# Kernel optimization log

Measured on AMD Instinct MI355X. Metric: run time of the kernel, lower is better.

The kernel has to match this reference:

```python
import jax, jax.numpy as jnp
import numpy as np
from jax import lax

NEG = -1e9
B, H, C, TX, TY = 4, 256, 80, 256, 1024  # batch, hidden, mel bins, text len, mel len


def setup_inputs() -> dict:
    key = jax.random.key(0)
    k = jax.random.split(key, 6)
    en = jax.random.normal(k[0], (B, H, TX), jnp.float32)
    mu = jax.random.normal(k[1], (B, C, TX), jnp.float32)
    log_sigma = 0.1 * jax.random.normal(k[2], (B, C, TX), jnp.float32)
    y = jax.random.normal(k[3], (B, C, TY), jnp.float32)
    x_lengths = jax.random.randint(k[4], (B,), TX // 2, TX + 1, jnp.int32)
    y_lengths = jax.random.randint(k[5], (B,), TY // 2, TY + 1, jnp.int32)
    return {"en": en, "mu": mu, "log_sigma": log_sigma, "y": y,
            "x_lengths": x_lengths, "y_lengths": y_lengths}


def sequence_mask(lengths, max_len):
    return jnp.arange(max_len)[None, :] < lengths[:, None]


def compute_log_probs(mu, log_sigma, y):
    # y: [B,C,Ty] -> [B,1,Ty,C]; mu/log_sigma: [B,C,Tx] -> [B,Tx,1,C]
    yb = jnp.transpose(y, (0, 2, 1))[:, None]
    mub = jnp.transpose(mu, (0, 2, 1))[:, :, None]
    lsb = jnp.transpose(log_sigma, (0, 2, 1))[:, :, None]
    # mse / sigma^2 = (y-mu)^2 * exp(-2*log_sigma); mean over channel dim
    expo = -0.5 * jnp.mean((yb - mub) ** 2 * jnp.exp(-2.0 * lsb), axis=-1)  # [B,Tx,Ty]
    return expo - 0.5 * jnp.mean(lsb, axis=-1)  # broadcast [B,Tx,1] -> [B,Tx,Ty]


def maximum_path(logp, mask, x_lengths, y_lengths):
    """Monotonic alignment search (Glow-TTS Viterbi DP), vectorized over batch."""
    b, tx, ty = logp.shape
    lp = jnp.where(mask > 0, logp, NEG)
    cols = jnp.moveaxis(lp, 2, 0)  # [Ty, B, Tx]
    v0 = jnp.broadcast_to(jnp.where(jnp.arange(tx) == 0, 0.0, NEG), (b, tx)).astype(logp.dtype)

    def fwd(v, col):
        v_shift = jnp.concatenate([jnp.full((b, 1), NEG, v.dtype), v[:, :-1]], axis=1)
        diag = v_shift > v  # come from (x-1, y-1) rather than (x, y-1)
        return col + jnp.maximum(v, v_shift), diag

    _, diags = lax.scan(fwd, v0, cols)  # diags: [Ty, B, Tx] bool

    xs_idx = jnp.arange(tx)

    def bwd(idx, inp):
        yv, dcol = inp
        active = yv < y_lengths  # [B]
        row = (xs_idx[None, :] == idx[:, None]) & active[:, None]
        d = jnp.take_along_axis(dcol, idx[:, None], axis=1)[:, 0]
        idx = jnp.where(active & (idx > 0) & d, idx - 1, idx)
        return idx, row

    _, rows = lax.scan(bwd, x_lengths - 1, (jnp.arange(ty), diags), reverse=True)
    return lax.stop_gradient(jnp.moveaxis(rows, 0, 2).astype(logp.dtype))  # [B,Tx,Ty]


def generate_path(dr, mask):
    # dr: [B,Tx] durations; mask: [B,Tx,Ty]
    ty = mask.shape[-1]
    cum = jnp.cumsum(dr, axis=1)
    pm = (jnp.arange(ty)[None, None, :] < cum[:, :, None]).astype(dr.dtype)
    path = pm - jnp.pad(pm, ((0, 0), (1, 0), (0, 0)))[:, :-1]
    return path * mask


def reference(en, mu, log_sigma, y, x_lengths, y_lengths):
    tx, ty = mu.shape[-1], y.shape[-1]
    x_mask = sequence_mask(x_lengths, tx).astype(jnp.float32)  # [B,Tx]
    y_mask = sequence_mask(y_lengths, ty).astype(jnp.float32)  # [B,Ty]
    attn_mask = x_mask[:, :, None] * y_mask[:, None, :]        # [B,Tx,Ty]
    logp = compute_log_probs(mu, log_sigma, y)
    attn = maximum_path(logp, attn_mask, x_lengths, y_lengths)
    dr_mas = jnp.sum(attn, axis=-1)                            # durations [B,Tx]
    path = generate_path(dr_mas, attn_mask)                    # convert_dr_to_align
    # expand_encoder_outputs: attn^T @ en^T -> [B,H,Ty]
    o_en_ex = jnp.einsum('bxy,bhx->bhy', path, en)
    return o_en_ex, logp, attn, dr_mas
```

## Files before the change

### kernel.cpp

```cpp
#include <hip/hip_runtime.h>
#include <cstdint>
#include <cmath>

#define B_ 4
#define H_ 256
#define C_ 80
#define TX_ 256
#define TY_ 1024
#define NEGF (-1e9f)

#define OFF_LOGP (B_*H_*TY_)
#define OFF_ATTN (OFF_LOGP + B_*TX_*TY_)
#define OFF_DR   (OFF_ATTN + B_*TX_*TY_)

__device__ __forceinline__ float dpp_shr1_negfill_f32(float x) {
  union { float f; int i; } u, o, r;
  u.f = x; o.f = NEGF;
  r.i = __builtin_amdgcn_update_dpp(o.i, u.i, 0x138, 0xf, 0xf, false);
  return r.f;
}

__global__ __launch_bounds__(256) void k_logp(
    const float* __restrict__ mu, const float* __restrict__ ls,
    const float* __restrict__ y, const int* __restrict__ xlp,
    const int* __restrict__ ylp, float* __restrict__ logp_out,
    float* __restrict__ lpT)
{
  const int b  = blockIdx.z;
  const int tq = blockIdx.y;
  const int x0 = blockIdx.x * 4;
  const int tid = threadIdx.x;
  const int lane = tid & 63;
  const int xi = tid >> 6;

  __shared__ double2 s_wm[4][C_];
  __shared__ double  s_wm2[4][C_];
  __shared__ double  s_lsv[4][C_];
  __shared__ double  s_K[4];
  __shared__ double  s_t0[4];
  __shared__ float   tile[256][4];

  for (int i = tid; i < 4 * C_; i += 256) {
    int xj = i / C_, c = i - xj * C_;
    double m = (double)mu[(b * C_ + c) * TX_ + x0 + xj];
    double l = (double)ls[(b * C_ + c) * TX_ + x0 + xj];
    double w = exp(-2.0 * l);
    s_wm[xj][c]  = make_double2(w, -2.0 * w * m);
    s_wm2[xj][c] = w * m * m;
    s_lsv[xj][c] = l;
  }
  __syncthreads();
  {
    int cc = lane;
    double kp = (cc < C_) ? s_wm2[xi][cc] : 0.0;
    double tp = (cc < C_) ? s_lsv[xi][cc] : 0.0;
    if (cc + 64 < C_) { kp += s_wm2[xi][cc + 64]; tp += s_lsv[xi][cc + 64]; }
#pragma unroll
    for (int off = 32; off; off >>= 1) {
      kp += __shfl_down(kp, off);
      tp += __shfl_down(tp, off);
    }
    if (cc == 0) { s_K[xi] = kp; s_t0[xi] = -0.5 * (tp * (1.0 / C_)); }
  }
  __syncthreads();

  double acc[4];
#pragma unroll
  for (int k = 0; k < 4; ++k) acc[k] = 0.0;

  const float4* yp = (const float4*)(y + (size_t)b * C_ * TY_ + tq * 256) + lane;
#pragma unroll 4
  for (int c = 0; c < C_; ++c) {
    float4 yv = yp[c * (TY_ / 4)];
    double y0 = yv.x, y1 = yv.y, y2 = yv.z, y3 = yv.w;
    double2 wm = s_wm[xi][c];
    double w = wm.x, m1 = wm.y;
    double u0 = fma(w, y0, m1), u1 = fma(w, y1, m1);
    double u2 = fma(w, y2, m1), u3 = fma(w, y3, m1);
    acc[0] = fma(u0, y0, acc[0]);
    acc[1] = fma(u1, y1, acc[1]);
    acc[2] = fma(u2, y2, acc[2]);
    acc[3] = fma(u3, y3, acc[3]);
  }

  const int xlen = xlp[b], ylen = ylp[b];
  const int x  = x0 + xi;
  const int t0 = tq * 256 + lane * 4;
  {
    double c0 = s_t0[xi], K = s_K[xi];
    float r[4];
#pragma unroll
    for (int k = 0; k < 4; ++k)
      r[k] = (float)((acc[k] + K) * (-0.5 / C_) + c0);
    *(float4*)&logp_out[((size_t)(b * TX_ + x)) * TY_ + t0] =
        make_float4(r[0], r[1], r[2], r[3]);
    bool xm = x < xlen;
#pragma unroll
    for (int k = 0; k < 4; ++k)
      tile[lane * 4 + k][xi] = (xm && (t0 + k) < ylen) ? r[k] : NEGF;
  }
  __syncthreads();

  float* dst = lpT + (size_t)b * TY_ * TX_ + x0;
  const float4* tp = (const float4*)tile;
  *(float4*)&dst[(size_t)(tq * 256 + tid) * TX_] = tp[tid];
}

#define POLL_FLAG(i)                                                     \
  { while (vflag[i] == 0u) __builtin_amdgcn_s_sleep(1);                  \
    asm volatile("" ::: "memory"); }

#define DP_CHUNK(SHBASE)                                                 \
  _Pragma("unroll")                                                      \
  for (int u = 0; u < 16; ++u) {                                         \
    float4 col = rr[u & 7];                                              \
    rr[u & 7] = (u < 8) ? pA[(u + 8) * 64 + lane]                        \
                        : pB[(u - 8) * 64 + lane];                       \
    float sh = dpp_shr1_negfill_f32(v3);                                 \
    float m0 = fmaxf(v0, sh);                                            \
    float m1 = fmaxf(v1, v0);                                            \
    float m2 = fmaxf(v2, v1);                                            \
    float m3 = fmaxf(v3, v2);                                            \
    w0 |= (__float_as_uint(v0 - m0) >> 31) << ((SHBASE) + u);            \
    w1 |= (__float_as_uint(v1 - m1) >> 31) << ((SHBASE) + u);            \
    w2 |= (__float_as_uint(v2 - m2) >> 31) << ((SHBASE) + u);            \
    w3 |= (__float_as_uint(v3 - m3) >> 31) << ((SHBASE) + u);            \
    v0 = col.x + m0;                                                     \
    v1 = col.y + m1;                                                     \
    v2 = col.z + m2;                                                     \
    v3 = col.w + m3;                                                     \
  }

__global__ __launch_bounds__(256, 1) void k_dp(
    const float* __restrict__ lpT, const int* __restrict__ xlp,
    const int* __restrict__ ylp, float* __restrict__ dr_out,
    int* __restrict__ cum_ws, int* __restrict__ xt_ws)
{
  const int b = blockIdx.x;
  const int tid = threadIdx.x;
  const int lane = tid & 63;
  const int w = tid >> 6;
  __shared__ __align__(16) float    ring[6 * 16 * 256];
  __shared__ __align__(16) uint32_t bits[8192];
  __shared__ __align__(16) uint32_t dur[TX_];
  __shared__ uint32_t flags[64];
  __shared__ int      prog;

  const float4* gb4   = (const float4*)(lpT + (size_t)b * TY_ * TX_);
  const float4* ring4 = (const float4*)ring;

  const int ylen = ylp[b];
  const int nch  = ((ylen + 31) >> 5) << 1;

  if (tid < 64) flags[tid] = 0u;
  if (tid == 0) prog = -1;
  __syncthreads();

  if (w == 0) {
    volatile uint32_t* vflag = flags;
    volatile int*      vprog = &prog;
    POLL_FLAG(0);
    float4 rr[8];
#pragma unroll
    for (int i = 0; i < 8; ++i) rr[i] = ring4[i * 64 + lane];

    float v0 = (lane == 0) ? 0.0f : NEGF;
    float v1 = NEGF, v2 = NEGF, v3 = NEGF;
    uint32_t w0 = 0, w1 = 0, w2 = 0, w3 = 0;
    int sA = 0, sB = 1;
    const float4* pA;
    const float4* pB;

    for (int cp = 0; cp < nch; cp += 2) {
      { int nf = (cp + 1 < nch) ? cp + 1 : nch - 1; POLL_FLAG(nf); }
      pA = ring4 + sA * 1024; pB = ring4 + sB * 1024;
      DP_CHUNK(0)
      asm volatile("" ::: "memory");
      *vprog = cp;
      sA = sB; sB = (sB == 5) ? 0 : sB + 1;

      { int nf = (cp + 2 < nch) ? cp + 2 : nch - 1; POLL_FLAG(nf); }
      pA = ring4 + sA * 1024; pB = ring4 + sB * 1024;
      DP_CHUNK(16)
      *(uint4*)&bits[(cp >> 1) * 256 + 4 * lane] = make_uint4(w0, w1, w2, w3);
      w0 = w1 = w2 = w3 = 0;
      asm volatile("" ::: "memory");
      *vprog = cp + 1;
      sA = sB; sB = (sB == 5) ? 0 : sB + 1;
    }
  } else {
    const int p = w - 1;
    volatile int*      vprog = &prog;
    volatile uint32_t* vflag = flags;
    for (int c = p; c < nch; c += 3) {
      const int need = c - 6;
      while (*vprog < need) __builtin_amdgcn_s_sleep(8);
      asm volatile("" ::: "memory");
      const float4* src = gb4 + (size_t)(c * 16) * 64 + lane;
      float4 tmp[16];
#pragma unroll
      for (int r = 0; r < 16; ++r) tmp[r] = src[r * 64];
      float4* dst = (float4*)&ring[(c % 6) * 4096] + lane;
#pragma unroll
      for (int r = 0; r < 16; ++r) dst[r * 64] = tmp[r];
      asm volatile("s_waitcnt lgkmcnt(0)" ::: "memory");
      vflag[c] = 1u;
    }
  }

  __syncthreads();
  dur[tid] = 0;
  __syncthreads();

  const int xlen = xlp[b];
  if (tid == 0) {
    int idx = xlen - 1;
    int t = ylen - 1;
    while (t >= 0) {
      if (idx == 0) { dur[0] = (uint32_t)(t + 1); break; }
      int ww = t >> 5, rrm = t & 31;
      uint32_t wd = bits[ww * 256 + idx];
      wd &= (rrm == 31) ? 0xffffffffu : ((1u << (rrm + 1)) - 1u);
      while (wd == 0 && ww > 0) { --ww; wd = bits[ww * 256 + idx]; }
      if (wd == 0) { dur[idx] = (uint32_t)(t + 1); break; }
      int bitpos = 31 - __builtin_clz(wd);
      int tp = (ww << 5) | bitpos;
      dur[idx] = (uint32_t)(t - tp + 1);
      --idx;
      t = tp - 1;
    }
  }
  __syncthreads();

  if (w == 0) {
    uint32_t d0 = dur[4 * lane], d1 = dur[4 * lane + 1];
    uint32_t d2 = dur[4 * lane + 2], d3 = dur[4 * lane + 3];
    uint32_t own = d0 + d1 + d2 + d3;
    uint32_t s = own;
#pragma unroll
    for (int off = 1; off < 64; off <<= 1) {
      uint32_t n = __shfl_up(s, off);
      if (lane >= off) s += n;
    }
    uint32_t base = s - own;
    uint32_t c0 = base + d0, c1 = c0 + d1, c2 = c1 + d2, c3 = c2 + d3;
    int x = 4 * lane;
    cum_ws[b * TX_ + x]     = (int)c0;
    cum_ws[b * TX_ + x + 1] = (int)c1;
    cum_ws[b * TX_ + x + 2] = (int)c2;
    cum_ws[b * TX_ + x + 3] = (int)c3;
    dr_out[b * TX_ + x]     = (float)d0;
    dr_out[b * TX_ + x + 1] = (float)d1;
    dr_out[b * TX_ + x + 2] = (float)d2;
    dr_out[b * TX_ + x + 3] = (float)d3;
    int* xt = xt_ws + b * TY_;
    for (uint32_t t = c0 - d0; t < c0; ++t) xt[t] = x;
    for (uint32_t t = c1 - d1; t < c1; ++t) xt[t] = x + 1;
    for (uint32_t t = c2 - d2; t < c2; ++t) xt[t] = x + 2;
    for (uint32_t t = c3 - d3; t < c3; ++t) xt[t] = x + 3;
  }
}

__global__ __launch_bounds__(256) void k_epi(
    const int* __restrict__ cum_ws, const int* __restrict__ xt_ws,
    const float* __restrict__ en, const int* __restrict__ ylp,
    float* __restrict__ attn, float* __restrict__ oen)
{
  const int b = blockIdx.y, bx = blockIdx.x, tid = threadIdx.x;
  __shared__ float row[TX_];
  if (bx < TX_) {
    const int x = bx;
    int hi = cum_ws[b * TX_ + x];
    int lo = (x > 0) ? cum_ws[b * TX_ + x - 1] : 0;
    int t0 = tid * 4;
    float4 v;
    v.x = (t0     >= lo && t0     < hi) ? 1.f : 0.f;
    v.y = (t0 + 1 >= lo && t0 + 1 < hi) ? 1.f : 0.f;
    v.z = (t0 + 2 >= lo && t0 + 2 < hi) ? 1.f : 0.f;
    v.w = (t0 + 3 >= lo && t0 + 3 < hi) ? 1.f : 0.f;
    *(float4*)&attn[((size_t)(b * TX_ + x)) * TY_ + t0] = v;
  } else {
    const int h = bx - TX_;
    row[tid] = en[((size_t)(b * H_ + h)) * TX_ + tid];
    __syncthreads();
    const int ylen = ylp[b];
    int t0 = tid * 4;
    int4 xi = *(const int4*)&xt_ws[b * TY_ + t0];
    float4 v;
    v.x = (t0     < ylen) ? row[xi.x & (TX_ - 1)] : 0.f;
    v.y = (t0 + 1 < ylen) ? row[xi.y & (TX_ - 1)] : 0.f;
    v.z = (t0 + 2 < ylen) ? row[xi.z & (TX_ - 1)] : 0.f;
    v.w = (t0 + 3 < ylen) ? row[xi.w & (TX_ - 1)] : 0.f;
    *(float4*)&oen[((size_t)(b * H_ + h)) * TY_ + t0] = v;
  }
}

extern "C" void kernel_launch(void* const* d_in, const int* in_sizes, int n_in,
                              void* d_out, int out_size, void* d_ws, size_t ws_size,
                              hipStream_t stream)
{
  const float* en = (const float*)d_in[0];
  const float* mu = (const float*)d_in[1];
  const float* ls = (const float*)d_in[2];
  const float* y  = (const float*)d_in[3];
  const int*   xl = (const int*)d_in[4];
  const int*   yl = (const int*)d_in[5];

  float* out  = (float*)d_out;
  float* oen  = out;
  float* logp = out + OFF_LOGP;
  float* attn = out + OFF_ATTN;
  float* dr   = out + OFF_DR;

  int* cum = (int*)d_ws;
  int* xt  = cum + B_ * TX_;

  k_logp<<<dim3(TX_ / 4, TY_ / 256, B_), 256, 0, stream>>>(mu, ls, y, xl, yl, logp, attn);
  k_dp  <<<B_,                           256, 0, stream>>>(attn, xl, yl, dr, cum, xt);
  k_epi <<<dim3(TX_ + H_, B_),           256, 0, stream>>>(cum, xt, en, yl, attn, oen);
}
```

Baseline: 166.7 us.

## Halve logp tile width, vectorize mu/ls loads, cache backtrack bit strips

The logp kernel now processes 128 time steps per block instead of 256, doubling the grid and halving per-thread FP64 accumulators, so more waves run concurrently. The mu/log_sigma staging uses float4 loads per channel instead of scalar strided loads. The serial backtrack in the DP kernel caches a uint4 strip of bit words and reuses it when consecutive steps hit the same word group, cutting dependent single-thread loads. The cost is that each block reloads and recomputes the per-channel weights twice as often.

```diff
diff --git a/kernel.cpp b/kernel.cpp
--- a/kernel.cpp
+++ b/kernel.cpp
@@ -38,16 +38,22 @@
   __shared__ double  s_lsv[4][C_];
   __shared__ double  s_K[4];
   __shared__ double  s_t0[4];
-  __shared__ float   tile[256][4];
-
-  for (int i = tid; i < 4 * C_; i += 256) {
-    int xj = i / C_, c = i - xj * C_;
-    double m = (double)mu[(b * C_ + c) * TX_ + x0 + xj];
-    double l = (double)ls[(b * C_ + c) * TX_ + x0 + xj];
-    double w = exp(-2.0 * l);
-    s_wm[xj][c]  = make_double2(w, -2.0 * w * m);
-    s_wm2[xj][c] = w * m * m;
-    s_lsv[xj][c] = l;
+  __shared__ float   tile[128][4];
+
+  for (int c = tid; c < C_; c += 256) {
+    float4 m4 = *(const float4*)&mu[(b * C_ + c) * TX_ + x0];
+    float4 l4 = *(const float4*)&ls[(b * C_ + c) * TX_ + x0];
+    const float mv[4] = {m4.x, m4.y, m4.z, m4.w};
+    const float lv[4] = {l4.x, l4.y, l4.z, l4.w};
+#pragma unroll
+    for (int xj = 0; xj < 4; ++xj) {
+      double m = (double)mv[xj];
+      double l = (double)lv[xj];
+      double w = exp(-2.0 * l);
+      s_wm[xj][c]  = make_double2(w, -2.0 * w * m);
+      s_wm2[xj][c] = w * m * m;
+      s_lsv[xj][c] = l;
+    }
   }
   __syncthreads();
   {
@@ -64,46 +70,37 @@
   }
   __syncthreads();
 
-  double acc[4];
-#pragma unroll
-  for (int k = 0; k < 4; ++k) acc[k] = 0.0;
-
-  const float4* yp = (const float4*)(y + (size_t)b * C_ * TY_ + tq * 256) + lane;
+  double acc0 = 0.0, acc1 = 0.0;
+  const float2* yp = (const float2*)(y + (size_t)b * C_ * TY_ + tq * 128) + lane;
 #pragma unroll 4
   for (int c = 0; c < C_; ++c) {
-    float4 yv = yp[c * (TY_ / 4)];
-    double y0 = yv.x, y1 = yv.y, y2 = yv.z, y3 = yv.w;
+    float2 yv = yp[c * (TY_ / 2)];
+    double y0 = yv.x, y1 = yv.y;
     double2 wm = s_wm[xi][c];
     double w = wm.x, m1 = wm.y;
     double u0 = fma(w, y0, m1), u1 = fma(w, y1, m1);
-    double u2 = fma(w, y2, m1), u3 = fma(w, y3, m1);
-    acc[0] = fma(u0, y0, acc[0]);
-    acc[1] = fma(u1, y1, acc[1]);
-    acc[2] = fma(u2, y2, acc[2]);
-    acc[3] = fma(u3, y3, acc[3]);
+    acc0 = fma(u0, y0, acc0);
+    acc1 = fma(u1, y1, acc1);
   }
 
   const int xlen = xlp[b], ylen = ylp[b];
   const int x  = x0 + xi;
-  const int t0 = tq * 256 + lane * 4;
+  const int t0 = tq * 128 + lane * 2;
   {
     double c0 = s_t0[xi], K = s_K[xi];
-    float r[4];
-#pragma unroll
-    for (int k = 0; k < 4; ++k)
-      r[k] = (float)((acc[k] + K) * (-0.5 / C_) + c0);
-    *(float4*)&logp_out[((size_t)(b * TX_ + x)) * TY_ + t0] =
-        make_float4(r[0], r[1], r[2], r[3]);
+    float r0 = (float)((acc0 + K) * (-0.5 / C_) + c0);
+    float r1 = (float)((acc1 + K) * (-0.5 / C_) + c0);
+    *(float2*)&logp_out[((size_t)(b * TX_ + x)) * TY_ + t0] = make_float2(r0, r1);
     bool xm = x < xlen;
-#pragma unroll
-    for (int k = 0; k < 4; ++k)
-      tile[lane * 4 + k][xi] = (xm && (t0 + k) < ylen) ? r[k] : NEGF;
-  }
-  __syncthreads();
-
-  float* dst = lpT + (size_t)b * TY_ * TX_ + x0;
-  const float4* tp = (const float4*)tile;
-  *(float4*)&dst[(size_t)(tq * 256 + tid) * TX_] = tp[tid];
+    tile[lane * 2    ][xi] = (xm && (t0    ) < ylen) ? r0 : NEGF;
+    tile[lane * 2 + 1][xi] = (xm && (t0 + 1) < ylen) ? r1 : NEGF;
+  }
+  __syncthreads();
+
+  if (tid < 128) {
+    float* dst = lpT + (size_t)b * TY_ * TX_ + x0;
+    *(float4*)&dst[(size_t)(tq * 128 + tid) * TX_] = ((const float4*)tile)[tid];
+  }
 }
 
 #define POLL_FLAG(i)                                                     \
@@ -216,12 +213,29 @@
   if (tid == 0) {
     int idx = xlen - 1;
     int t = ylen - 1;
+    int cww = -2, cbase = -2;
+    uint4 strip = make_uint4(0u, 0u, 0u, 0u);
     while (t >= 0) {
       if (idx == 0) { dur[0] = (uint32_t)(t + 1); break; }
       int ww = t >> 5, rrm = t & 31;
-      uint32_t wd = bits[ww * 256 + idx];
+      int base = idx & ~3;
+      if (ww != cww || base != cbase) {
+        strip = *(const uint4*)&bits[ww * 256 + base];
+        cww = ww; cbase = base;
+      }
+      const int sel = idx & 3;
+      uint32_t wd = (sel == 0) ? strip.x
+                  : (sel == 1) ? strip.y
+                  : (sel == 2) ? strip.z : strip.w;
       wd &= (rrm == 31) ? 0xffffffffu : ((1u << (rrm + 1)) - 1u);
-      while (wd == 0 && ww > 0) { --ww; wd = bits[ww * 256 + idx]; }
+      while (wd == 0 && ww > 0) {
+        --ww;
+        strip = *(const uint4*)&bits[ww * 256 + base];
+        cww = ww;
+        wd = (sel == 0) ? strip.x
+           : (sel == 1) ? strip.y
+           : (sel == 2) ? strip.z : strip.w;
+      }
       if (wd == 0) { dur[idx] = (uint32_t)(t + 1); break; }
       int bitpos = 31 - __builtin_clz(wd);
       int tp = (ww << 5) | bitpos;
@@ -315,7 +329,7 @@
   int* cum = (int*)d_ws;
   int* xt  = cum + B_ * TX_;
 
-  k_logp<<<dim3(TX_ / 4, TY_ / 256, B_), 256, 0, stream>>>(mu, ls, y, xl, yl, logp, attn);
+  k_logp<<<dim3(TX_ / 4, TY_ / 128, B_), 256, 0, stream>>>(mu, ls, y, xl, yl, logp, attn);
   k_dp  <<<B_,                           256, 0, stream>>>(attn, xl, yl, dr, cum, xt);
   k_epi <<<dim3(TX_ + H_, B_),           256, 0, stream>>>(cum, xt, en, yl, attn, oen);
 }
```

Result: slower. 177.2 us (+6.3%).
